# Kernel optimization log

Measured on AMD Instinct MI355X. Metric: run time of the kernel, lower is better.

## Reference

```python
import jax, jax.numpy as jnp
import numpy as np

NUM_HEADS = 16

def setup_inputs() -> dict:
    key = jax.random.key(0)
    k1, k2, k3 = jax.random.split(key, 3)
    B, N, C = 2, 2048, 1024
    x = jax.random.normal(k1, (B, N, C), dtype=jnp.float32)
    w_qkv = jax.random.normal(k2, (C, 3 * C), dtype=jnp.float32) * (C ** -0.5)
    w_proj = jax.random.normal(k3, (C, C), dtype=jnp.float32) * (C ** -0.5)
    b_proj = jnp.zeros((C,), dtype=jnp.float32)
    return {"x": x, "w_qkv": w_qkv, "w_proj": w_proj, "b_proj": b_proj}

def reference(x, w_qkv, w_proj, b_proj):
    B, N, C = x.shape
    H = NUM_HEADS
    D = C // H
    scale = D ** -0.5
    qkv = (x @ w_qkv).reshape(B, N, 3, H, D).transpose(2, 0, 3, 1, 4)  # [3,B,H,N,D]
    q, k, v = qkv[0], qkv[1], qkv[2]
    attn = jnp.einsum("bhnd,bhmd->bhnm", q, k) * scale  # [B,H,N,N]
    attn = jax.nn.softmax(attn, axis=-1)
    out = jnp.einsum("bhnm,bhmd->bhnd", attn, v)  # [B,H,N,D]
    out = out.transpose(0, 2, 1, 3).reshape(B, N, C)
    return out @ w_proj + b_proj
```

## Files before the change

### kernel.cpp

```cpp
#include <hip/hip_runtime.h>
#include <hip/hip_bf16.h>
#include <math.h>

#define B_SZ   2
#define N_SEQ  2048
#define C_DIM  1024
#define H_NUM  16
#define D_HEAD 64
#define M_ROWS (B_SZ * N_SEQ)
#define QKV_N  (3 * C_DIM)

typedef __attribute__((ext_vector_type(8))) short  bf16x8;
typedef __attribute__((ext_vector_type(4))) float  floatx4;

static __device__ __forceinline__ unsigned short f2bf(float x) {
    unsigned int u = __float_as_uint(x);
    u = (u + 0x7FFFu + ((u >> 16) & 1u)) >> 16;
    return (unsigned short)u;
}
static __device__ __forceinline__ unsigned int f2bf_hi(float x) {
    unsigned int u = __float_as_uint(x);
    return u + 0x7FFFu + ((u >> 16) & 1u);
}
#if __has_builtin(__builtin_amdgcn_cvt_pk_bf16_f32)
typedef __bf16 bf16_2 __attribute__((ext_vector_type(2)));
static __device__ __forceinline__ unsigned int pkbf(float a, float b) {
    union { bf16_2 v; unsigned int u; } c;
    c.v = __builtin_amdgcn_cvt_pk_bf16_f32(a, b);
    return c.u;
}
#else
static __device__ __forceinline__ unsigned int pkbf(float a, float b) {
    return __builtin_amdgcn_perm(f2bf_hi(b), f2bf_hi(a), 0x07060302u);
}
#endif

#if __has_builtin(__builtin_amdgcn_exp2f)
#define EXP2F(x) __builtin_amdgcn_exp2f(x)
#else
#define EXP2F(x) exp2f(x)
#endif

#define GLP(p) ((const __attribute__((address_space(1))) void*)(p))
#define LDP(p) ((__attribute__((address_space(3))) void*)(p))

#define CEXP 0.18033688011112042f

__global__ __launch_bounds__(256)
void prep_fused(const float* __restrict__ x,      unsigned short* __restrict__ xb,
                const float* __restrict__ w_qkv,  unsigned short* __restrict__ wqkvT,
                const float* __restrict__ w_proj, unsigned short* __restrict__ wprojT)
{
    __shared__ unsigned short t[64][72];
    const int bid = blockIdx.x;
    const int tid = threadIdx.x;

    if (bid < 4096) {
        const int i = bid * 256 + tid;
        float4 v = ((const float4*)x)[i];
        ushort4 p;
        p.x = f2bf(v.x); p.y = f2bf(v.y); p.z = f2bf(v.z); p.w = f2bf(v.w);
        ((ushort4*)xb)[i] = p;
        return;
    }

    const float* W;
    unsigned short* WT;
    int N, tt;
    if (bid < 4096 + 768) { W = w_qkv;  WT = wqkvT;  N = QKV_N; tt = bid - 4096; }
    else                  { W = w_proj; WT = wprojT; N = C_DIM; tt = bid - 4864; }
    const int ntiles = N / 64;
    const int n0 = (tt % ntiles) * 64;
    const int k0 = (tt / ntiles) * 64;
    const int K  = C_DIM;

    const int tc = tid & 15;
    const int tr = tid >> 4;
    #pragma unroll
    for (int p = 0; p < 4; ++p) {
        const int r = tr + p * 16;
        float4 v = *(const float4*)&W[(size_t)(k0 + r) * N + n0 + tc * 4];
        ushort4 pk;
        pk.x = f2bf(v.x); pk.y = f2bf(v.y); pk.z = f2bf(v.z); pk.w = f2bf(v.w);
        *(ushort4*)&t[r][tc * 4] = pk;
    }
    __syncthreads();

    const int n  = tid >> 2;
    const int c0 = (tid & 3) * 16;
    unsigned short tmp[16];
    #pragma unroll
    for (int i = 0; i < 16; ++i) tmp[i] = t[c0 + i][n];
    *(uint4*)&WT[(size_t)(n0 + n) * K + k0 + c0]     = *(uint4*)&tmp[0];
    *(uint4*)&WT[(size_t)(n0 + n) * K + k0 + c0 + 8] = *(uint4*)&tmp[8];
}

__global__ __launch_bounds__(256)
void gemm_qkv(const unsigned short* __restrict__ A,
              const unsigned short* __restrict__ BT,
              unsigned short* __restrict__ qbuf,
              unsigned short* __restrict__ kbuf,
              unsigned short* __restrict__ vbuf)
{
    const int K = C_DIM;
    __shared__ unsigned short As[128 * 64];
    __shared__ unsigned short Bs[128 * 64];

    const int tid  = threadIdx.x;
    const int lane = tid & 63;
    const int wave = tid >> 6;
    const int l15  = lane & 15;
    const int lq   = lane >> 4;
    const int e7   = l15 & 7;
    const int wm   = (wave & 1) * 64;
    const int wn   = (wave >> 1) * 64;

    const int bid = blockIdx.x;
    const int xcd = bid & 7;
    const int j   = bid >> 3;
    const int bm  = (j / 3) * 128;
    const int bn  = ((j % 3) * 8 + xcd) * 128;

    const int srow = tid >> 3;
    const int gso  = ((tid & 7) ^ (srow & 7)) * 8;

    const unsigned short* ga = A  + (size_t)(bm + srow) * K + gso;
    const unsigned short* gb = BT + (size_t)(bn + srow) * K + gso;

    floatx4 acc[4][4];
    #pragma unroll
    for (int i = 0; i < 4; ++i)
        #pragma unroll
        for (int jj = 0; jj < 4; ++jj) acc[i][jj] = (floatx4){0.f, 0.f, 0.f, 0.f};

    for (int kt = 0; kt < K; kt += 64) {
        #pragma unroll
        for (int i = 0; i < 4; ++i) {
            __builtin_amdgcn_global_load_lds(GLP(ga + (size_t)i * 32 * K + kt),
                                             LDP(&As[i * 2048 + tid * 8]), 16, 0, 0);
            __builtin_amdgcn_global_load_lds(GLP(gb + (size_t)i * 32 * K + kt),
                                             LDP(&Bs[i * 2048 + tid * 8]), 16, 0, 0);
        }
        __syncthreads();

        bf16x8 af[2][4], bfr[2][4];
        #pragma unroll
        for (int t = 0; t < 4; ++t) {
            #pragma unroll
            for (int kc = 0; kc < 2; ++kc) {
                af[kc][t]  = *(const bf16x8*)&As[(wm + t * 16 + l15) * 64
                                                 + (((kc * 4 + lq) ^ e7) * 8)];
                bfr[kc][t] = *(const bf16x8*)&Bs[(wn + t * 16 + l15) * 64
                                                 + (((kc * 4 + lq) ^ e7) * 8)];
            }
        }
        #pragma unroll
        for (int kc = 0; kc < 2; ++kc)
            #pragma unroll
            for (int mt = 0; mt < 4; ++mt)
                #pragma unroll
                for (int nt = 0; nt < 4; ++nt)
                    acc[mt][nt] = __builtin_amdgcn_mfma_f32_16x16x32_bf16(
                        af[kc][mt], bfr[kc][nt], acc[mt][nt], 0, 0, 0);
        __syncthreads();
    }

    #pragma unroll
    for (int nt = 0; nt < 4; ++nt) {
        const int col  = bn + wn + nt * 16 + l15;
        const int reg3 = col >> 10;
        const int h    = (col >> 6) & 15;
        const int d    = col & 63;
        const float sc4 = (reg3 == 0) ? CEXP : 1.0f;
        #pragma unroll
        for (int mt = 0; mt < 4; ++mt) {
            const int row = bm + wm + mt * 16 + lq * 4;
            const int b   = row >> 11;
            const int n   = row & 2047;
            if (reg3 < 2) {
                unsigned short* dst = (reg3 ? kbuf : qbuf)
                    + ((size_t)(b * H_NUM + h) * N_SEQ + n) * D_HEAD + d;
                #pragma unroll
                for (int r = 0; r < 4; ++r)
                    dst[(size_t)r * D_HEAD] = f2bf(acc[mt][nt][r] * sc4);
            } else {
                const int a  = n & 63;
                const int fk = (a & 0x20) | ((a & 0x0C) << 1) | ((a & 0x10) >> 2);
                unsigned short* dst = vbuf
                    + ((size_t)(b * H_NUM + h) * D_HEAD + d) * N_SEQ + (n & ~63) + fk;
                ushort4 pk;
                pk.x = f2bf(acc[mt][nt][0]); pk.y = f2bf(acc[mt][nt][1]);
                pk.z = f2bf(acc[mt][nt][2]); pk.w = f2bf(acc[mt][nt][3]);
                *(ushort4*)dst = pk;
            }
        }
    }
}

__global__ __launch_bounds__(512, 4)
void attn_mfma(const unsigned short* __restrict__ qbuf,
               const unsigned short* __restrict__ kbuf,
               const unsigned short* __restrict__ vbuf,
               unsigned short* __restrict__ attnb)
{
    __shared__ unsigned short KsS[2][2][64 * 64];
    __shared__ unsigned short VtS[2][2][64 * 64];

    const int tid  = threadIdx.x;
    const int lane = tid & 63;
    const int wave = tid >> 6;
    const int grp  = wave >> 2;
    const int wrow = wave & 3;
    const int l15  = lane & 15;
    const int lq   = lane >> 4;
    const int e    = l15 & 7;

    const int bid  = blockIdx.x;
    const int bh   = (bid & 7) * 4 + (bid >> 7);
    const int qblk = (bid >> 3) & 15;
    const int b    = bh >> 4;
    const int h    = bh & 15;
    const int q0   = qblk * 128 + wrow * 32;

    const unsigned short* khead = kbuf + (size_t)bh * N_SEQ * D_HEAD;
    const unsigned short* vhead = vbuf + (size_t)bh * D_HEAD * N_SEQ;

    bf16x8 qf[2][2];
    #pragma unroll
    for (int qb = 0; qb < 2; ++qb) {
        const unsigned short* qrow = qbuf
            + ((size_t)bh * N_SEQ + q0 + qb * 16 + l15) * D_HEAD + lq * 8;
        qf[0][qb] = *(const bf16x8*)qrow;
        qf[1][qb] = *(const bf16x8*)(qrow + 32);
    }

    floatx4 acc[4][2];
    #pragma unroll
    for (int dc = 0; dc < 4; ++dc)
        #pragma unroll
        for (int qb = 0; qb < 2; ++qb) acc[dc][qb] = (floatx4){0.f, 0.f, 0.f, 0.f};
    float lsum[2] = {0.f, 0.f};

    const int srow = tid >> 3;
    const int gso  = ((tid & 7) ^ (srow & 7)) * 8;

    #pragma unroll
    for (int i = 0; i < 2; ++i) {
        __builtin_amdgcn_global_load_lds(GLP(khead + (size_t)(i * 64 + srow) * 64 + gso),
                                         LDP(&KsS[0][i][tid * 8]), 16, 0, 0);
        __builtin_amdgcn_global_load_lds(GLP(vhead + (size_t)srow * N_SEQ + i * 64 + gso),
                                         LDP(&VtS[0][i][tid * 8]), 16, 0, 0);
    }

    for (int s = 0; s < N_SEQ / 128; ++s) {
        const int cur = s & 1;
        __syncthreads();

        if (s + 1 < N_SEQ / 128) {
            const int m1 = (s + 1) * 128;
            const int nx = cur ^ 1;
            #pragma unroll
            for (int i = 0; i < 2; ++i) {
                __builtin_amdgcn_global_load_lds(
                    GLP(khead + (size_t)(m1 + i * 64 + srow) * 64 + gso),
                    LDP(&KsS[nx][i][tid * 8]), 16, 0, 0);
                __builtin_amdgcn_global_load_lds(
                    GLP(vhead + (size_t)srow * N_SEQ + m1 + i * 64 + gso),
                    LDP(&VtS[nx][i][tid * 8]), 16, 0, 0);
            }
        }

        const unsigned short* Ksc = &KsS[cur][grp][0];
        const unsigned short* Vtc = &VtS[cur][grp][0];

        floatx4 st[4][2];
        #pragma unroll
        for (int t = 0; t < 4; ++t) {
            bf16x8 k0 = *(const bf16x8*)&Ksc[(t * 16 + l15) * 64 + ((lq ^ e) * 8)];
            bf16x8 k1 = *(const bf16x8*)&Ksc[(t * 16 + l15) * 64 + (((4 + lq) ^ e) * 8)];
            #pragma unroll
            for (int qb = 0; qb < 2; ++qb) {
                floatx4 sv = (floatx4){-8.f, -8.f, -8.f, -8.f};
                sv = __builtin_amdgcn_mfma_f32_16x16x32_bf16(k0, qf[0][qb], sv, 0, 0, 0);
                sv = __builtin_amdgcn_mfma_f32_16x16x32_bf16(k1, qf[1][qb], sv, 0, 0, 0);
                st[t][qb] = sv;
            }
        }

        bf16x8 pf[2][2];
        #pragma unroll
        for (int qb = 0; qb < 2; ++qb) {
            unsigned int pk[8];
            float la = 0.f;
            #pragma unroll
            for (int t = 0; t < 4; ++t) {
                float p0 = EXP2F(st[t][qb][0]);
                float p1 = EXP2F(st[t][qb][1]);
                float p2 = EXP2F(st[t][qb][2]);
                float p3 = EXP2F(st[t][qb][3]);
                la += (p0 + p1) + (p2 + p3);
                pk[t * 2]     = pkbf(p0, p1);
                pk[t * 2 + 1] = pkbf(p2, p3);
            }
            lsum[qb] += la;
            union { uint4 u; bf16x8 v; } c0, c1;
            c0.u = make_uint4(pk[0], pk[1], pk[2], pk[3]);
            c1.u = make_uint4(pk[4], pk[5], pk[6], pk[7]);
            pf[0][qb] = c0.v;
            pf[1][qb] = c1.v;
        }

        #pragma unroll
        for (int dc = 0; dc < 4; ++dc) {
            bf16x8 v0 = *(const bf16x8*)&Vtc[(dc * 16 + l15) * 64 + ((lq ^ e) * 8)];
            bf16x8 v1 = *(const bf16x8*)&Vtc[(dc * 16 + l15) * 64 + (((4 + lq) ^ e) * 8)];
            #pragma unroll
            for (int qb = 0; qb < 2; ++qb) {
                acc[dc][qb] = __builtin_amdgcn_mfma_f32_16x16x32_bf16(
                    v0, pf[0][qb], acc[dc][qb], 0, 0, 0);
                acc[dc][qb] = __builtin_amdgcn_mfma_f32_16x16x32_bf16(
                    v1, pf[1][qb], acc[dc][qb], 0, 0, 0);
            }
        }
    }

    __syncthreads();
    float* smA = (float*)&KsS[0][0][0];
    float* smL = (float*)&VtS[0][0][0];
    const int li = wrow * 64 + lane;
    if (grp) {
        float* p = smA + li * 32;
        #pragma unroll
        for (int dc = 0; dc < 4; ++dc)
            #pragma unroll
            for (int qb = 0; qb < 2; ++qb)
                #pragma unroll
                for (int r = 0; r < 4; ++r)
                    p[(dc * 8 + qb * 4 + r) ^ (lane & 31)] = acc[dc][qb][r];
        smL[li * 2]     = lsum[0];
        smL[li * 2 + 1] = lsum[1];
    }
    __syncthreads();
    if (grp) return;

    {
        const float* p = smA + li * 32;
        #pragma unroll
        for (int dc = 0; dc < 4; ++dc)
            #pragma unroll
            for (int qb = 0; qb < 2; ++qb)
                #pragma unroll
                for (int r = 0; r < 4; ++r)
                    acc[dc][qb][r] += p[(dc * 8 + qb * 4 + r) ^ (lane & 31)];
        lsum[0] += smL[li * 2];
        lsum[1] += smL[li * 2 + 1];
    }

    #pragma unroll
    for (int qb = 0; qb < 2; ++qb) {
        float l = lsum[qb];
        l += __shfl_xor(l, 16, 64);
        l += __shfl_xor(l, 32, 64);
        const float inv = 1.f / l;
        const int q = q0 + qb * 16 + l15;
        unsigned short* orow = attnb + ((size_t)b * N_SEQ + q) * C_DIM + h * D_HEAD;
        #pragma unroll
        for (int dc = 0; dc < 4; ++dc) {
            ushort4 pkk;
            pkk.x = f2bf(acc[dc][qb][0] * inv);
            pkk.y = f2bf(acc[dc][qb][1] * inv);
            pkk.z = f2bf(acc[dc][qb][2] * inv);
            pkk.w = f2bf(acc[dc][qb][3] * inv);
            *(ushort4*)&orow[dc * 16 + lq * 4] = pkk;
        }
    }
}

__global__ __launch_bounds__(256)
void gemm_bt(const unsigned short* __restrict__ A,
             const unsigned short* __restrict__ BT,
             const float* __restrict__ bias,
             float* __restrict__ Cm,
             int M, int N, int K)
{
    __shared__ unsigned short As[128 * 64];
    __shared__ unsigned short Bs[64 * 64];

    const int tid  = threadIdx.x;
    const int lane = tid & 63;
    const int wave = tid >> 6;
    const int l15  = lane & 15;
    const int lq   = lane >> 4;
    const int e7   = l15 & 7;
    const int wm   = (wave & 1) * 64;
    const int wn   = (wave >> 1) * 32;

    const int bid = blockIdx.x;
    const int xcd = bid & 7;
    const int j   = bid >> 3;
    const int bm  = (j >> 1) * 128;
    const int bn  = ((j & 1) * 8 + xcd) * 64;

    const int srow = tid >> 3;
    const int gso  = ((tid & 7) ^ (srow & 7)) * 8;

    const unsigned short* ga = A  + (size_t)(bm + srow) * K + gso;
    const unsigned short* gb = BT + (size_t)(bn + srow) * K + gso;

    floatx4 acc[4][2];
    #pragma unroll
    for (int i = 0; i < 4; ++i)
        #pragma unroll
        for (int jj = 0; jj < 2; ++jj) acc[i][jj] = (floatx4){0.f, 0.f, 0.f, 0.f};

    for (int kt = 0; kt < K; kt += 64) {
        #pragma unroll
        for (int i = 0; i < 4; ++i)
            __builtin_amdgcn_global_load_lds(GLP(ga + (size_t)i * 32 * K + kt),
                                             LDP(&As[i * 2048 + tid * 8]), 16, 0, 0);
        #pragma unroll
        for (int i = 0; i < 2; ++i)
            __builtin_amdgcn_global_load_lds(GLP(gb + (size_t)i * 32 * K + kt),
                                             LDP(&Bs[i * 2048 + tid * 8]), 16, 0, 0);
        __syncthreads();

        bf16x8 af[2][4], bfr[2][2];
        #pragma unroll
        for (int t = 0; t < 4; ++t)
            #pragma unroll
            for (int kc = 0; kc < 2; ++kc)
                af[kc][t] = *(const bf16x8*)&As[(wm + t * 16 + l15) * 64
                                                + (((kc * 4 + lq) ^ e7) * 8)];
        #pragma unroll
        for (int t = 0; t < 2; ++t)
            #pragma unroll
            for (int kc = 0; kc < 2; ++kc)
                bfr[kc][t] = *(const bf16x8*)&Bs[(wn + t * 16 + l15) * 64
                                                 + (((kc * 4 + lq) ^ e7) * 8)];
        #pragma unroll
        for (int kc = 0; kc < 2; ++kc)
            #pragma unroll
            for (int mt = 0; mt < 4; ++mt)
                #pragma unroll
                for (int nt = 0; nt < 2; ++nt)
                    acc[mt][nt] = __builtin_amdgcn_mfma_f32_16x16x32_bf16(
                        af[kc][mt], bfr[kc][nt], acc[mt][nt], 0, 0, 0);
        __syncthreads();
    }

    float bv[2];
    #pragma unroll
    for (int nt = 0; nt < 2; ++nt) bv[nt] = bias[bn + wn + nt * 16 + l15];
    #pragma unroll
    for (int mt = 0; mt < 4; ++mt) {
        const int row = bm + wm + mt * 16 + lq * 4;
        #pragma unroll
        for (int nt = 0; nt < 2; ++nt) {
            const int col = bn + wn + nt * 16 + l15;
            #pragma unroll
            for (int r = 0; r < 4; ++r)
                Cm[(size_t)(row + r) * N + col] = acc[mt][nt][r] + bv[nt];
        }
    }
}

extern "C" void kernel_launch(void* const* d_in, const int* in_sizes, int n_in,
                              void* d_out, int out_size, void* d_ws, size_t ws_size,
                              hipStream_t stream)
{
    const float* x      = (const float*)d_in[0];
    const float* w_qkv  = (const float*)d_in[1];
    const float* w_proj = (const float*)d_in[2];
    const float* b_proj = (const float*)d_in[3];
    float*       out    = (float*)d_out;

    unsigned short* xb     = (unsigned short*)d_ws;
    unsigned short* wqkvT  = xb     + (size_t)M_ROWS * C_DIM;
    unsigned short* wprojT = wqkvT  + (size_t)QKV_N * C_DIM;
    unsigned short* qbuf   = wprojT + (size_t)C_DIM * C_DIM;
    unsigned short* kbuf   = qbuf   + (size_t)M_ROWS * C_DIM;
    unsigned short* vbuf   = kbuf   + (size_t)M_ROWS * C_DIM;
    unsigned short* attnb  = vbuf   + (size_t)M_ROWS * C_DIM;

    prep_fused<<<4096 + 768 + 256, 256, 0, stream>>>(x, xb, w_qkv, wqkvT, w_proj, wprojT);

    gemm_qkv<<<768, 256, 0, stream>>>(xb, wqkvT, qbuf, kbuf, vbuf);

    attn_mfma<<<512, 512, 0, stream>>>(qbuf, kbuf, vbuf, attnb);

    gemm_bt<<<512, 256, 0, stream>>>(attnb, wprojT, b_proj, out, M_ROWS, C_DIM, C_DIM);
}
```

Before: 185.2 us.

## Software-pipeline PV MFMAs one iteration behind QK and softmax in attention loop

The attention inner loop now keeps the V fragments and bf16 probabilities in registers and issues the PV MFMAs for the previous tile at the start of the next iteration, with a drain step after the loop. The aim is to overlap the PV matrix work with the next tile's QK MFMAs and exp computation, and s_setprio raises wave priority around the MFMA bursts. V is read from LDS before the exp work so the read latency is hidden. The cost is extra live registers (vf, pfp), which may lower occupancy or cause spills.

New measurement: 210.8 us. +13.8%, slower.

```diff
diff --git a/kernel.cpp b/kernel.cpp
--- a/kernel.cpp
+++ b/kernel.cpp
@@ -241,6 +241,16 @@
         for (int qb = 0; qb < 2; ++qb) acc[dc][qb] = (floatx4){0.f, 0.f, 0.f, 0.f};
     float lsum[2] = {0.f, 0.f};
 
+    bf16x8 vf[2][4];
+    bf16x8 pfp[2][2];
+    #pragma unroll
+    for (int i = 0; i < 2; ++i) {
+        #pragma unroll
+        for (int dc = 0; dc < 4; ++dc) vf[i][dc] = (bf16x8){0,0,0,0,0,0,0,0};
+        #pragma unroll
+        for (int qb = 0; qb < 2; ++qb) pfp[i][qb] = (bf16x8){0,0,0,0,0,0,0,0};
+    }
+
     const int srow = tid >> 3;
     const int gso  = ((tid & 7) ^ (srow & 7)) * 8;
 
@@ -270,6 +280,20 @@
             }
         }
 
+        if (s) {
+            __builtin_amdgcn_s_setprio(1);
+            #pragma unroll
+            for (int dc = 0; dc < 4; ++dc)
+                #pragma unroll
+                for (int qb = 0; qb < 2; ++qb) {
+                    acc[dc][qb] = __builtin_amdgcn_mfma_f32_16x16x32_bf16(
+                        vf[0][dc], pfp[0][qb], acc[dc][qb], 0, 0, 0);
+                    acc[dc][qb] = __builtin_amdgcn_mfma_f32_16x16x32_bf16(
+                        vf[1][dc], pfp[1][qb], acc[dc][qb], 0, 0, 0);
+                }
+            __builtin_amdgcn_s_setprio(0);
+        }
+
         const unsigned short* Ksc = &KsS[cur][grp][0];
         const unsigned short* Vtc = &VtS[cur][grp][0];
 
@@ -287,7 +311,12 @@
             }
         }
 
-        bf16x8 pf[2][2];
+        #pragma unroll
+        for (int dc = 0; dc < 4; ++dc) {
+            vf[0][dc] = *(const bf16x8*)&Vtc[(dc * 16 + l15) * 64 + ((lq ^ e) * 8)];
+            vf[1][dc] = *(const bf16x8*)&Vtc[(dc * 16 + l15) * 64 + (((4 + lq) ^ e) * 8)];
+        }
+
         #pragma unroll
         for (int qb = 0; qb < 2; ++qb) {
             unsigned int pk[8];
@@ -306,22 +335,23 @@
             union { uint4 u; bf16x8 v; } c0, c1;
             c0.u = make_uint4(pk[0], pk[1], pk[2], pk[3]);
             c1.u = make_uint4(pk[4], pk[5], pk[6], pk[7]);
-            pf[0][qb] = c0.v;
-            pf[1][qb] = c1.v;
-        }
-
-        #pragma unroll
-        for (int dc = 0; dc < 4; ++dc) {
-            bf16x8 v0 = *(const bf16x8*)&Vtc[(dc * 16 + l15) * 64 + ((lq ^ e) * 8)];
-            bf16x8 v1 = *(const bf16x8*)&Vtc[(dc * 16 + l15) * 64 + (((4 + lq) ^ e) * 8)];
+            pfp[0][qb] = c0.v;
+            pfp[1][qb] = c1.v;
+        }
+    }
+
+    {
+        __builtin_amdgcn_s_setprio(1);
+        #pragma unroll
+        for (int dc = 0; dc < 4; ++dc)
             #pragma unroll
             for (int qb = 0; qb < 2; ++qb) {
                 acc[dc][qb] = __builtin_amdgcn_mfma_f32_16x16x32_bf16(
-                    v0, pf[0][qb], acc[dc][qb], 0, 0, 0);
+                    vf[0][dc], pfp[0][qb], acc[dc][qb], 0, 0, 0);
                 acc[dc][qb] = __builtin_amdgcn_mfma_f32_16x16x32_bf16(
-                    v1, pf[1][qb], acc[dc][qb], 0, 0, 0);
+                    vf[1][dc], pfp[1][qb], acc[dc][qb], 0, 0, 0);
             }
-        }
+        __builtin_amdgcn_s_setprio(0);
     }
 
     __syncthreads();
```

## Double-buffer LDS tiles in QKV and projection GEMMs to overlap loads with MFMA

Applied to the files above, without the earlier changes.

Both GEMM kernels now keep two LDS buffers for the A and B tiles. The first K-tile is loaded before the loop, and each iteration prefetches the next tile into the other buffer while MFMAs run on the current one. This also drops the trailing barrier, leaving one barrier per iteration. The cost is double the LDS footprint per block, and the compiler may still insert vmcnt waits that serialize the direct-to-LDS loads.

Measured after the change: 194.7 us. 5.1% more time.

```diff
diff --git a/kernel.cpp b/kernel.cpp
--- a/kernel.cpp
+++ b/kernel.cpp
@@ -103,8 +103,8 @@
               unsigned short* __restrict__ vbuf)
 {
     const int K = C_DIM;
-    __shared__ unsigned short As[128 * 64];
-    __shared__ unsigned short Bs[128 * 64];
+    __shared__ unsigned short As[2][128 * 64];
+    __shared__ unsigned short Bs[2][128 * 64];
 
     const int tid  = threadIdx.x;
     const int lane = tid & 63;
@@ -133,24 +133,38 @@
         #pragma unroll
         for (int jj = 0; jj < 4; ++jj) acc[i][jj] = (floatx4){0.f, 0.f, 0.f, 0.f};
 
-    for (int kt = 0; kt < K; kt += 64) {
-        #pragma unroll
-        for (int i = 0; i < 4; ++i) {
-            __builtin_amdgcn_global_load_lds(GLP(ga + (size_t)i * 32 * K + kt),
-                                             LDP(&As[i * 2048 + tid * 8]), 16, 0, 0);
-            __builtin_amdgcn_global_load_lds(GLP(gb + (size_t)i * 32 * K + kt),
-                                             LDP(&Bs[i * 2048 + tid * 8]), 16, 0, 0);
-        }
+    #pragma unroll
+    for (int i = 0; i < 4; ++i) {
+        __builtin_amdgcn_global_load_lds(GLP(ga + (size_t)i * 32 * K),
+                                         LDP(&As[0][i * 2048 + tid * 8]), 16, 0, 0);
+        __builtin_amdgcn_global_load_lds(GLP(gb + (size_t)i * 32 * K),
+                                         LDP(&Bs[0][i * 2048 + tid * 8]), 16, 0, 0);
+    }
+
+    for (int it = 0; it < K / 64; ++it) {
+        const int cur = it & 1;
         __syncthreads();
 
+        if (it + 1 < K / 64) {
+            const int kt1 = (it + 1) * 64;
+            const int nx  = cur ^ 1;
+            #pragma unroll
+            for (int i = 0; i < 4; ++i) {
+                __builtin_amdgcn_global_load_lds(GLP(ga + (size_t)i * 32 * K + kt1),
+                                                 LDP(&As[nx][i * 2048 + tid * 8]), 16, 0, 0);
+                __builtin_amdgcn_global_load_lds(GLP(gb + (size_t)i * 32 * K + kt1),
+                                                 LDP(&Bs[nx][i * 2048 + tid * 8]), 16, 0, 0);
+            }
+        }
+
         bf16x8 af[2][4], bfr[2][4];
         #pragma unroll
         for (int t = 0; t < 4; ++t) {
             #pragma unroll
             for (int kc = 0; kc < 2; ++kc) {
-                af[kc][t]  = *(const bf16x8*)&As[(wm + t * 16 + l15) * 64
+                af[kc][t]  = *(const bf16x8*)&As[cur][(wm + t * 16 + l15) * 64
                                                  + (((kc * 4 + lq) ^ e7) * 8)];
-                bfr[kc][t] = *(const bf16x8*)&Bs[(wn + t * 16 + l15) * 64
+                bfr[kc][t] = *(const bf16x8*)&Bs[cur][(wn + t * 16 + l15) * 64
                                                  + (((kc * 4 + lq) ^ e7) * 8)];
             }
         }
@@ -162,7 +176,6 @@
                 for (int nt = 0; nt < 4; ++nt)
                     acc[mt][nt] = __builtin_amdgcn_mfma_f32_16x16x32_bf16(
                         af[kc][mt], bfr[kc][nt], acc[mt][nt], 0, 0, 0);
-        __syncthreads();
     }
 
     #pragma unroll
@@ -383,8 +396,8 @@
              float* __restrict__ Cm,
              int M, int N, int K)
 {
-    __shared__ unsigned short As[128 * 64];
-    __shared__ unsigned short Bs[64 * 64];
+    __shared__ unsigned short As[2][128 * 64];
+    __shared__ unsigned short Bs[2][64 * 64];
 
     const int tid  = threadIdx.x;
     const int lane = tid & 63;
@@ -413,29 +426,44 @@
         #pragma unroll
         for (int jj = 0; jj < 2; ++jj) acc[i][jj] = (floatx4){0.f, 0.f, 0.f, 0.f};
 
-    for (int kt = 0; kt < K; kt += 64) {
-        #pragma unroll
-        for (int i = 0; i < 4; ++i)
-            __builtin_amdgcn_global_load_lds(GLP(ga + (size_t)i * 32 * K + kt),
-                                             LDP(&As[i * 2048 + tid * 8]), 16, 0, 0);
-        #pragma unroll
-        for (int i = 0; i < 2; ++i)
-            __builtin_amdgcn_global_load_lds(GLP(gb + (size_t)i * 32 * K + kt),
-                                             LDP(&Bs[i * 2048 + tid * 8]), 16, 0, 0);
+    #pragma unroll
+    for (int i = 0; i < 4; ++i)
+        __builtin_amdgcn_global_load_lds(GLP(ga + (size_t)i * 32 * K),
+                                         LDP(&As[0][i * 2048 + tid * 8]), 16, 0, 0);
+    #pragma unroll
+    for (int i = 0; i < 2; ++i)
+        __builtin_amdgcn_global_load_lds(GLP(gb + (size_t)i * 32 * K),
+                                         LDP(&Bs[0][i * 2048 + tid * 8]), 16, 0, 0);
+
+    for (int it = 0; it < K / 64; ++it) {
+        const int cur = it & 1;
         __syncthreads();
 
+        if (it + 1 < K / 64) {
+            const int kt1 = (it + 1) * 64;
+            const int nx  = cur ^ 1;
+            #pragma unroll
+            for (int i = 0; i < 4; ++i)
+                __builtin_amdgcn_global_load_lds(GLP(ga + (size_t)i * 32 * K + kt1),
+                                                 LDP(&As[nx][i * 2048 + tid * 8]), 16, 0, 0);
+            #pragma unroll
+            for (int i = 0; i < 2; ++i)
+                __builtin_amdgcn_global_load_lds(GLP(gb + (size_t)i * 32 * K + kt1),
+                                                 LDP(&Bs[nx][i * 2048 + tid * 8]), 16, 0, 0);
+        }
+
         bf16x8 af[2][4], bfr[2][2];
         #pragma unroll
         for (int t = 0; t < 4; ++t)
             #pragma unroll
             for (int kc = 0; kc < 2; ++kc)
-                af[kc][t] = *(const bf16x8*)&As[(wm + t * 16 + l15) * 64
+                af[kc][t] = *(const bf16x8*)&As[cur][(wm + t * 16 + l15) * 64
                                                 + (((kc * 4 + lq) ^ e7) * 8)];
         #pragma unroll
         for (int t = 0; t < 2; ++t)
             #pragma unroll
             for (int kc = 0; kc < 2; ++kc)
-                bfr[kc][t] = *(const bf16x8*)&Bs[(wn + t * 16 + l15) * 64
+                bfr[kc][t] = *(const bf16x8*)&Bs[cur][(wn + t * 16 + l15) * 64
                                                  + (((kc * 4 + lq) ^ e7) * 8)];
         #pragma unroll
         for (int kc = 0; kc < 2; ++kc)
@@ -445,7 +473,6 @@
                 for (int nt = 0; nt < 2; ++nt)
                     acc[mt][nt] = __builtin_amdgcn_mfma_f32_16x16x32_bf16(
                         af[kc][mt], bfr[kc][nt], acc[mt][nt], 0, 0, 0);
-        __syncthreads();
     }
 
     float bv[2];
```

## Load K/V tiles directly from global into registers, dropping LDS staging

Applied to the files above, without the earlier changes.

The attention kernel no longer stages K and V tiles through double-buffered shared memory with async global-to-LDS loads and a per-iteration barrier. Each wave now reads its own K and V fragments straight from global memory into registers. This removes the barriers and LDS traffic, and shrinks shared memory to only the final reduction buffers. In exchange, the four waves sharing a group each re-read the same K/V data from global or L2, and there is no explicit prefetch, so global-load latency is exposed.

Result: slower. 258.6 us (+39.6%).

```diff
diff --git a/kernel.cpp b/kernel.cpp
--- a/kernel.cpp
+++ b/kernel.cpp
@@ -203,8 +203,8 @@
                const unsigned short* __restrict__ vbuf,
                unsigned short* __restrict__ attnb)
 {
-    __shared__ unsigned short KsS[2][2][64 * 64];
-    __shared__ unsigned short VtS[2][2][64 * 64];
+    __shared__ float smA[4 * 64 * 32];
+    __shared__ float smL[256 * 2];
 
     const int tid  = threadIdx.x;
     const int lane = tid & 63;
@@ -213,7 +213,6 @@
     const int wrow = wave & 3;
     const int l15  = lane & 15;
     const int lq   = lane >> 4;
-    const int e    = l15 & 7;
 
     const int bid  = blockIdx.x;
     const int bh   = (bid & 7) * 4 + (bid >> 7);
@@ -241,50 +240,37 @@
         for (int qb = 0; qb < 2; ++qb) acc[dc][qb] = (floatx4){0.f, 0.f, 0.f, 0.f};
     float lsum[2] = {0.f, 0.f};
 
-    const int srow = tid >> 3;
-    const int gso  = ((tid & 7) ^ (srow & 7)) * 8;
-
-    #pragma unroll
-    for (int i = 0; i < 2; ++i) {
-        __builtin_amdgcn_global_load_lds(GLP(khead + (size_t)(i * 64 + srow) * 64 + gso),
-                                         LDP(&KsS[0][i][tid * 8]), 16, 0, 0);
-        __builtin_amdgcn_global_load_lds(GLP(vhead + (size_t)srow * N_SEQ + i * 64 + gso),
-                                         LDP(&VtS[0][i][tid * 8]), 16, 0, 0);
-    }
-
     for (int s = 0; s < N_SEQ / 128; ++s) {
-        const int cur = s & 1;
-        __syncthreads();
-
-        if (s + 1 < N_SEQ / 128) {
-            const int m1 = (s + 1) * 128;
-            const int nx = cur ^ 1;
-            #pragma unroll
-            for (int i = 0; i < 2; ++i) {
-                __builtin_amdgcn_global_load_lds(
-                    GLP(khead + (size_t)(m1 + i * 64 + srow) * 64 + gso),
-                    LDP(&KsS[nx][i][tid * 8]), 16, 0, 0);
-                __builtin_amdgcn_global_load_lds(
-                    GLP(vhead + (size_t)srow * N_SEQ + m1 + i * 64 + gso),
-                    LDP(&VtS[nx][i][tid * 8]), 16, 0, 0);
-            }
-        }
-
-        const unsigned short* Ksc = &KsS[cur][grp][0];
-        const unsigned short* Vtc = &VtS[cur][grp][0];
+        const int m0 = s * 128 + grp * 64;
+        const unsigned short* kb = khead + (size_t)m0 * D_HEAD;
+        const unsigned short* vb = vhead + m0;
+
+        bf16x8 kk0[4], kk1[4];
+        #pragma unroll
+        for (int t = 0; t < 4; ++t) {
+            const unsigned short* kr = kb + (size_t)(t * 16 + l15) * D_HEAD + lq * 8;
+            kk0[t] = *(const bf16x8*)kr;
+            kk1[t] = *(const bf16x8*)(kr + 32);
+        }
 
         floatx4 st[4][2];
         #pragma unroll
         for (int t = 0; t < 4; ++t) {
-            bf16x8 k0 = *(const bf16x8*)&Ksc[(t * 16 + l15) * 64 + ((lq ^ e) * 8)];
-            bf16x8 k1 = *(const bf16x8*)&Ksc[(t * 16 + l15) * 64 + (((4 + lq) ^ e) * 8)];
             #pragma unroll
             for (int qb = 0; qb < 2; ++qb) {
                 floatx4 sv = (floatx4){-8.f, -8.f, -8.f, -8.f};
-                sv = __builtin_amdgcn_mfma_f32_16x16x32_bf16(k0, qf[0][qb], sv, 0, 0, 0);
-                sv = __builtin_amdgcn_mfma_f32_16x16x32_bf16(k1, qf[1][qb], sv, 0, 0, 0);
+                sv = __builtin_amdgcn_mfma_f32_16x16x32_bf16(kk0[t], qf[0][qb], sv, 0, 0, 0);
+                sv = __builtin_amdgcn_mfma_f32_16x16x32_bf16(kk1[t], qf[1][qb], sv, 0, 0, 0);
                 st[t][qb] = sv;
             }
+        }
+
+        bf16x8 vv0[4], vv1[4];
+        #pragma unroll
+        for (int dc = 0; dc < 4; ++dc) {
+            const unsigned short* vr = vb + (size_t)(dc * 16 + l15) * N_SEQ + lq * 8;
+            vv0[dc] = *(const bf16x8*)vr;
+            vv1[dc] = *(const bf16x8*)(vr + 32);
         }
 
         bf16x8 pf[2][2];
@@ -312,21 +298,17 @@
 
         #pragma unroll
         for (int dc = 0; dc < 4; ++dc) {
-            bf16x8 v0 = *(const bf16x8*)&Vtc[(dc * 16 + l15) * 64 + ((lq ^ e) * 8)];
-            bf16x8 v1 = *(const bf16x8*)&Vtc[(dc * 16 + l15) * 64 + (((4 + lq) ^ e) * 8)];
             #pragma unroll
             for (int qb = 0; qb < 2; ++qb) {
                 acc[dc][qb] = __builtin_amdgcn_mfma_f32_16x16x32_bf16(
-                    v0, pf[0][qb], acc[dc][qb], 0, 0, 0);
+                    vv0[dc], pf[0][qb], acc[dc][qb], 0, 0, 0);
                 acc[dc][qb] = __builtin_amdgcn_mfma_f32_16x16x32_bf16(
-                    v1, pf[1][qb], acc[dc][qb], 0, 0, 0);
+                    vv1[dc], pf[1][qb], acc[dc][qb], 0, 0, 0);
             }
         }
     }
 
     __syncthreads();
-    float* smA = (float*)&KsS[0][0][0];
-    float* smL = (float*)&VtS[0][0][0];
     const int li = wrow * 64 + lane;
     if (grp) {
         float* p = smA + li * 32;
```
